# Performance work log

Measured on AMD Instinct MI355X. Metric: run time of the kernel, lower is better.

The kernel has to match this reference:

```python
import jax, jax.numpy as jnp
import numpy as np

H, D = 4, 32  # num_heads, per-head out dim (out_feats=128)
N_AGENT, N_GT, N_UAV = 50000, 50000, 50000
E = 600000
IN = 64


def _gat(x_src, x_dst, src, dst, W_src, W_dst, al, ar, W_res, b, num_dst):
    """DGL-style bipartite GATConv with residual, bias and ReLU activation."""
    fs = (x_src @ W_src).reshape(-1, H, D)      # [Ns,H,D]
    fd = (x_dst @ W_dst).reshape(-1, H, D)      # [Nd,H,D]
    el = jnp.sum(fs * al, axis=-1)              # [Ns,H]
    er = jnp.sum(fd * ar, axis=-1)              # [Nd,H]
    e = jax.nn.leaky_relu(el[src] + er[dst], 0.2)          # [E,H]
    # segment softmax over incoming edges of each dst node
    emax = jax.ops.segment_max(e, dst, num_segments=num_dst)   # [Nd,H], -inf for deg-0
    ee = jnp.exp(e - emax[dst])
    denom = jax.ops.segment_sum(ee, dst, num_segments=num_dst)
    a = ee / denom[dst]                          # [E,H]
    msg = fs[src] * a[:, :, None]                # [E,H,D]
    rst = jax.ops.segment_sum(msg, dst, num_segments=num_dst)  # [Nd,H,D]; zeros for deg-0
    res = (x_dst @ W_res).reshape(-1, H, D)      # residual projection
    out = jax.nn.relu(rst + res + b.reshape(1, H, D))
    return out.reshape(num_dst, H * D)


def setup_inputs() -> dict:
    key = jax.random.key(0)
    ks = jax.random.split(key, 20)
    s = 0.1  # weight init scale
    return {
        'x_gt': jax.random.normal(ks[0], (N_GT, IN), jnp.float32),
        'x_uav': jax.random.normal(ks[1], (N_UAV, IN), jnp.float32),
        'x_agent': jax.random.normal(ks[2], (N_AGENT, IN), jnp.float32),
        'src_gt': jax.random.randint(ks[3], (E,), 0, N_GT, jnp.int32),
        'dst_gt': jax.random.randint(ks[4], (E,), 0, N_AGENT, jnp.int32),
        'src_uav': jax.random.randint(ks[5], (E,), 0, N_UAV, jnp.int32),
        'dst_uav': jax.random.randint(ks[6], (E,), 0, N_AGENT, jnp.int32),
        'W_src_gt': s * jax.random.normal(ks[7], (IN, H * D), jnp.float32),
        'W_dst_gt': s * jax.random.normal(ks[8], (IN, H * D), jnp.float32),
        'attn_l_gt': s * jax.random.normal(ks[9], (H, D), jnp.float32),
        'attn_r_gt': s * jax.random.normal(ks[10], (H, D), jnp.float32),
        'W_res_gt': s * jax.random.normal(ks[11], (IN, H * D), jnp.float32),
        'b_gt': jnp.zeros((H * D,), jnp.float32),
        'W_src_uav': s * jax.random.normal(ks[12], (IN, H * D), jnp.float32),
        'W_dst_uav': s * jax.random.normal(ks[13], (IN, H * D), jnp.float32),
        'attn_l_uav': s * jax.random.normal(ks[14], (H, D), jnp.float32),
        'attn_r_uav': s * jax.random.normal(ks[15], (H, D), jnp.float32),
        'W_res_uav': s * jax.random.normal(ks[16], (IN, H * D), jnp.float32),
        'b_uav': jnp.zeros((H * D,), jnp.float32),
        'W_f': s * jax.random.normal(ks[17], (2 * H * D, H * D), jnp.float32),
        'b_f': jnp.zeros((H * D,), jnp.float32),
    }


def reference(x_gt, x_uav, x_agent, src_gt, dst_gt, src_uav, dst_uav,
              W_src_gt, W_dst_gt, attn_l_gt, attn_r_gt, W_res_gt, b_gt,
              W_src_uav, W_dst_uav, attn_l_uav, attn_r_uav, W_res_uav, b_uav,
              W_f, b_f):
    h_gt = _gat(x_gt, x_agent, src_gt, dst_gt, W_src_gt, W_dst_gt,
                attn_l_gt, attn_r_gt, W_res_gt, b_gt, N_AGENT)
    h_uav = _gat(x_uav, x_agent, src_uav, dst_uav, W_src_uav, W_dst_uav,
                 attn_l_uav, attn_r_uav, W_res_uav, b_uav, N_AGENT)
    h = jnp.concatenate([h_gt, h_uav], axis=1)   # [N_agent, 256]
    return jax.nn.relu(h @ W_f + b_f)            # [N_agent, 128]
```

## Files before the change

kernel.cpp:

```cpp
#include <hip/hip_runtime.h>
#include <hip/hip_bf16.h>

using bf16 = __hip_bfloat16;

#define NA 50000
#define NE 600000

typedef __attribute__((ext_vector_type(8))) short short8;
typedef __attribute__((ext_vector_type(4))) float f32x4;

#define HBUF_B   0u
#define FS_B     25600000u
#define EL_B     51200000u
#define RECS_B   54400000u
#define CNT_B    68800000u
#define ROW_B    72000000u
#define TOPS_B   72400016u
#define FLAG_B   72400528u
#define WST_GT_B 72400544u
#define WST_UAV_B 72416928u
#define WRT_B    72433312u
#define WFT_B    72466080u
#define ELT_GT_B 72531616u
#define ELT_UAV_B 72533664u
#define ERT_B    72535712u
#define RANK_B   72537760u
#define WS_BYTES 77337760u

__device__ __forceinline__ float b2f(bf16 v) { return __bfloat162float(v); }

__device__ __forceinline__ float ldf(const void* p, size_t i, int f32) {
    return f32 ? ((const float*)p)[i] : b2f(((const bf16*)p)[i]);
}

__device__ __forceinline__ unsigned short f2bs(float v) {
    bf16 t = __float2bfloat16(v);
    return *(unsigned short*)&t;
}

__device__ __forceinline__ float lrelu_exp(float v) {
    v = v > 0.f ? v : 0.2f * v;
    return __expf(v);
}

__device__ __forceinline__ unsigned int pack_bf16x2(float a, float b) {
    return (unsigned int)f2bs(a) | ((unsigned int)f2bs(b) << 16);
}

__device__ __forceinline__ float lo_f(unsigned int u) { return __uint_as_float(u << 16); }
__device__ __forceinline__ float hi_f(unsigned int u) { return __uint_as_float(u & 0xffff0000u); }

__device__ __forceinline__ short8 ldfrag8(const void* p, size_t off, int f32) {
    if (!f32) return *(const short8*)((const unsigned short*)p + off);
    union { short8 s; unsigned int u[4]; } r;
    const float* fp = (const float*)p + off;
#pragma unroll
    for (int j = 0; j < 4; ++j) r.u[j] = pack_bf16x2(fp[2 * j], fp[2 * j + 1]);
    return r.s;
}

__device__ __forceinline__ unsigned int xcc_id() {
    unsigned int x;
    asm volatile("s_getreg_b32 %0, hwreg(HW_REG_XCC_ID)" : "=s"(x));
    return x & 7u;
}

__device__ int probe_f32(const void* x0) {
    __shared__ int cnt;
    if (threadIdx.x == 0) cnt = 0;
    __syncthreads();
    const bf16* p = (const bf16*)x0;
    int bad = 0;
    for (int i = threadIdx.x; i < 1024; i += 256) {
        float av = fabsf(b2f(p[i]));
        if (!(av <= 1e6f)) bad++;
    }
    if (bad) atomicAdd(&cnt, bad);
    __syncthreads();
    return cnt > 8;
}

__global__ void HeteroVisionConv_29703993819529_kernel(
    const void* x0,
    const void* Wsg, const void* alg, const void* Wdg, const void* arg_,
    const void* Wsu, const void* alu, const void* Wdu, const void* aru,
    const void* Wrg, const void* Wru, const void* Wf,
    unsigned short* wsT_gt, unsigned short* wsT_uav, unsigned short* wrT,
    unsigned short* wfT, unsigned short* elT_gt, unsigned short* elT_uav,
    unsigned short* erT,
    int* flag, unsigned int* outp, long sent) {
    int b = blockIdx.x, t = threadIdx.x;
    int f32 = probe_f32(x0);
    if (b == 20) {
        if (t == 0) { flag[0] = f32; outp[sent] = 0x447A447Au; }
        return;
    }
    if (b < 8) {
        for (int i = t; i < 16 * 256; i += 256) {
            int n = b * 16 + (i >> 8), k = i & 255;
            wfT[n * 256 + k] = f2bs(ldf(Wf, (size_t)k * 128 + n, f32));
        }
    } else if (b < 12) {
        for (int i = t; i < 64 * 64; i += 256) {
            int n = (b - 8) * 64 + (i >> 6), k = i & 63;
            float v = (n < 128) ? ldf(Wrg, (size_t)k * 128 + n, f32)
                                : ldf(Wru, (size_t)k * 128 + (n - 128), f32);
            wrT[n * 64 + k] = f2bs(v);
        }
    } else if (b < 14) {
        for (int i = t; i < 64 * 64; i += 256) {
            int n = (b - 12) * 64 + (i >> 6), k = i & 63;
            wsT_gt[n * 64 + k] = f2bs(ldf(Wsg, (size_t)k * 128 + n, f32));
        }
    } else if (b < 16) {
        for (int i = t; i < 64 * 64; i += 256) {
            int n = (b - 14) * 64 + (i >> 6), k = i & 63;
            wsT_uav[n * 64 + k] = f2bs(ldf(Wsu, (size_t)k * 128 + n, f32));
        }
    } else {
        int m = b - 16;
        const void* Wm = (m == 0) ? Wsg : (m == 1) ? Wdg : (m == 2) ? Wsu : Wdu;
        const void* Am = (m == 0) ? alg : (m == 1) ? arg_ : (m == 2) ? alu : aru;
        int k = t >> 2, h = t & 3;
        float a = 0.f;
        for (int d = 0; d < 32; ++d)
            a += ldf(Wm, (size_t)k * 128 + h * 32 + d, f32) *
                 ldf(Am, (size_t)h * 32 + d, f32);
        unsigned short v = f2bs(a);
        if (m == 0) {
            elT_gt[h * 64 + k] = v;
            for (int i = t; i < 12 * 64; i += 256) elT_gt[(4 + (i >> 6)) * 64 + (i & 63)] = 0;
        } else if (m == 2) {
            elT_uav[h * 64 + k] = v;
            for (int i = t; i < 12 * 64; i += 256) elT_uav[(4 + (i >> 6)) * 64 + (i & 63)] = 0;
        } else if (m == 1) {
            erT[h * 64 + k] = v;
        } else {
            erT[(4 + h) * 64 + k] = v;
            for (int i = t; i < 8 * 64; i += 256) erT[(8 + (i >> 6)) * 64 + (i & 63)] = 0;
        }
    }
}

__global__ void fused_k(const int* dg, const int* du,
                        unsigned int* cnt, unsigned int* rank,
                        const void* xg, const void* xu, const void* xa,
                        const unsigned short* wsT_gt, const unsigned short* wsT_uav,
                        const unsigned short* elT_gt, const unsigned short* elT_uav,
                        const unsigned short* wrT, const unsigned short* erT,
                        const void* bg, const void* bu,
                        float* elbase, bf16* fs, bf16* hbuf, const int* flag) {
    __shared__ unsigned short Bt[256 * 72];
    __shared__ float bl[256];
    int b = blockIdx.x, t = threadIdx.x;

    if (b < 3516 && (b % 3) == 0) {
        int idx = (b / 3) * 256 + t;
        if (idx >= 300000) return;
        int g = idx >= 150000;
        int e = (idx - g * 150000) * 4;
        int4 d4 = *(const int4*)((g ? du : dg) + e);
        unsigned int xcc = xcc_id();
        unsigned int* c = cnt + xcc * 100000 + g * NA;
        uint4 r4;
        r4.x = __hip_atomic_fetch_add(&c[d4.x], 1u, __ATOMIC_RELAXED,
                                      __HIP_MEMORY_SCOPE_WORKGROUP);
        r4.y = __hip_atomic_fetch_add(&c[d4.y], 1u, __ATOMIC_RELAXED,
                                      __HIP_MEMORY_SCOPE_WORKGROUP);
        r4.z = __hip_atomic_fetch_add(&c[d4.z], 1u, __ATOMIC_RELAXED,
                                      __HIP_MEMORY_SCOPE_WORKGROUP);
        r4.w = __hip_atomic_fetch_add(&c[d4.w], 1u, __ATOMIC_RELAXED,
                                      __HIP_MEMORY_SCOPE_WORKGROUP);
        unsigned int tag = xcc << 24;
        r4.x |= tag; r4.y |= tag; r4.z |= tag; r4.w |= tag;
        *(uint4*)(rank + (size_t)g * NE + e) = r4;
        return;
    }
    int nidx = (b < 3516) ? (b - b / 3 - 1) : (2344 + (b - 3516));
    int f32 = *flag;
    int lane = t & 63, w = t >> 6;
    int m = lane & 15, quad = lane >> 4;

    if (nidx < 1564) {
        int g = nidx / 782, bb = nidx % 782;
        const void* A = g ? xu : xg;
        const unsigned short* WT = g ? wsT_uav : wsT_gt;
        const unsigned short* ET = g ? elT_uav : elT_gt;
        float* elout = elbase + (g ? 400000 : 0);
        bf16* out = fs + (size_t)g * NA * 128;
        for (int i = t * 8; i < 128 * 64; i += 256 * 8) {
            short8 v = *(const short8*)(WT + i);
            int n = i >> 6, k = i & 63;
            *(short8*)&Bt[n * 72 + k] = v;
        }
        __syncthreads();
        int row = bb * 64 + w * 16 + m;
        int rowc = row < NA ? row : NA - 1;
        short8 a0 = ldfrag8(A, (size_t)rowc * 64 + quad * 8, f32);
        short8 a1 = ldfrag8(A, (size_t)rowc * 64 + 32 + quad * 8, f32);
        f32x4 acc[8];
#pragma unroll
        for (int nt = 0; nt < 8; ++nt) acc[nt] = (f32x4){0.f, 0.f, 0.f, 0.f};
#pragma unroll
        for (int nt = 0; nt < 8; ++nt) {
            short8 b0 = *(const short8*)&Bt[(nt * 16 + m) * 72 + quad * 8];
            short8 b1 = *(const short8*)&Bt[(nt * 16 + m) * 72 + 32 + quad * 8];
            acc[nt] = __builtin_amdgcn_mfma_f32_16x16x32_bf16(a0, b0, acc[nt], 0, 0, 0);
            acc[nt] = __builtin_amdgcn_mfma_f32_16x16x32_bf16(a1, b1, acc[nt], 0, 0, 0);
        }
        f32x4 eacc = (f32x4){0.f, 0.f, 0.f, 0.f};
        {
            short8 e0 = *(const short8*)&ET[m * 64 + quad * 8];
            short8 e1 = *(const short8*)&ET[m * 64 + 32 + quad * 8];
            eacc = __builtin_amdgcn_mfma_f32_16x16x32_bf16(a0, e0, eacc, 0, 0, 0);
            eacc = __builtin_amdgcn_mfma_f32_16x16x32_bf16(a1, e1, eacc, 0, 0, 0);
        }
        int srow = bb * 64 + w * 16 + quad * 4;
#pragma unroll
        for (int nt = 0; nt < 8; ++nt) {
#pragma unroll
            for (int r = 0; r < 4; ++r) {
                int rr = srow + r;
                if (rr < NA) out[(size_t)rr * 128 + nt * 16 + m] = __float2bfloat16(acc[nt][r]);
            }
        }
        if (m < 4) {
#pragma unroll
            for (int r = 0; r < 4; ++r) {
                int rr = srow + r;
                if (rr < NA) elout[(size_t)rr * 4 + m] = eacc[r];
            }
        }
        return;
    }
    int bb = nidx - 1564;
    for (int i = t * 8; i < 256 * 64; i += 256 * 8) {
        short8 v = *(const short8*)(wrT + i);
        int n = i >> 6, k = i & 63;
        *(short8*)&Bt[n * 72 + k] = v;
    }
    bl[t] = (t < 128) ? ldf(bg, t, f32) : ldf(bu, t - 128, f32);
    __syncthreads();
    int row = bb * 64 + w * 16 + m;
    int rowc = row < NA ? row : NA - 1;
    short8 a0 = ldfrag8(xa, (size_t)rowc * 64 + quad * 8, f32);
    short8 a1 = ldfrag8(xa, (size_t)rowc * 64 + 32 + quad * 8, f32);
    f32x4 acc[16];
#pragma unroll
    for (int nt = 0; nt < 16; ++nt) acc[nt] = (f32x4){0.f, 0.f, 0.f, 0.f};
#pragma unroll
    for (int nt = 0; nt < 16; ++nt) {
        short8 b0 = *(const short8*)&Bt[(nt * 16 + m) * 72 + quad * 8];
        short8 b1 = *(const short8*)&Bt[(nt * 16 + m) * 72 + 32 + quad * 8];
        acc[nt] = __builtin_amdgcn_mfma_f32_16x16x32_bf16(a0, b0, acc[nt], 0, 0, 0);
        acc[nt] = __builtin_amdgcn_mfma_f32_16x16x32_bf16(a1, b1, acc[nt], 0, 0, 0);
    }
    f32x4 eacc = (f32x4){0.f, 0.f, 0.f, 0.f};
    {
        short8 e0 = *(const short8*)&erT[m * 64 + quad * 8];
        short8 e1 = *(const short8*)&erT[m * 64 + 32 + quad * 8];
        eacc = __builtin_amdgcn_mfma_f32_16x16x32_bf16(a0, e0, eacc, 0, 0, 0);
        eacc = __builtin_amdgcn_mfma_f32_16x16x32_bf16(a1, e1, eacc, 0, 0, 0);
    }
    int srow = bb * 64 + w * 16 + quad * 4;
#pragma unroll
    for (int nt = 0; nt < 16; ++nt) {
        int col = nt * 16 + m;
#pragma unroll
        for (int r = 0; r < 4; ++r) {
            int rr = srow + r;
            if (rr < NA)
                hbuf[(size_t)rr * 256 + col] = __float2bfloat16(acc[nt][r] + bl[col]);
        }
    }
    if (m < 8) {
        float* ero = (m < 4) ? (elbase + 200000) : (elbase + 600000);
        int mm = m & 3;
#pragma unroll
        for (int r = 0; r < 4; ++r) {
            int rr = srow + r;
            if (rr < NA) ero[(size_t)rr * 4 + mm] = eacc[r];
        }
    }
}

__global__ void scan1_k(unsigned int* cnt, unsigned int* row, unsigned int* tops) {
    __shared__ unsigned int sh[256];
    int b = blockIdx.x, t = threadIdx.x;
    int base = b * 1024 + t * 4;
    unsigned int v[4];
    for (int j = 0; j < 4; ++j) {
        int d = base + j;
        unsigned int tot = 0u;
        if (d < 100000) {
#pragma unroll
            for (int x = 0; x < 8; ++x) {
                unsigned int c = cnt[x * 100000 + d];
                cnt[x * 100000 + d] = tot;
                tot += c;
            }
        }
        v[j] = tot;
    }
    unsigned int s = v[0] + v[1] + v[2] + v[3];
    sh[t] = s;
    __syncthreads();
    for (int off = 1; off < 256; off <<= 1) {
        unsigned int x = (t >= off) ? sh[t - off] : 0u;
        __syncthreads();
        sh[t] += x;
        __syncthreads();
    }
    unsigned int run = sh[t] - s;
    for (int j = 0; j < 4; ++j) {
        if (base + j < 100000) row[base + j] = run;
        run += v[j];
    }
    if (t == 255) tops[b] = sh[255];
}

__global__ void scan2_k(unsigned int* tops, unsigned int* row) {
    __shared__ unsigned int sh[128];
    int t = threadIdx.x;
    unsigned int v = (t < 98) ? tops[t] : 0u;
    sh[t] = v;
    __syncthreads();
    for (int off = 1; off < 128; off <<= 1) {
        unsigned int x = (t >= off) ? sh[t - off] : 0u;
        __syncthreads();
        sh[t] += x;
        __syncthreads();
    }
    if (t < 98) tops[t] = sh[t] - v;
    if (t == 97) row[100000] = sh[97];
}

__global__ void scan3_k(unsigned int* row, const unsigned int* tops) {
    int b = blockIdx.x, t = threadIdx.x;
    unsigned int off = tops[b];
    for (int i = b * 1024 + t; i < b * 1024 + 1024; i += 256) {
        if (i < 100000) row[i] += off;
    }
}

__global__ void scatter_k(const int* sg, const int* dg, const int* su, const int* du,
                          const float* elbase, const unsigned int* row,
                          const unsigned int* cnt, const unsigned int* rank,
                          unsigned int* recs) {
    int idx = blockIdx.x * 256 + threadIdx.x;
    if (idx >= 2 * NE) return;
    int g = idx >= NE;
    int e = idx - g * NE;
    int s = (g ? su : sg)[e];
    int d = (g ? du : dg)[e];
    const float4* el4 = (const float4*)(elbase + (g ? 400000 : 0));
    const float4* er4 = (const float4*)(elbase + (g ? 600000 : 200000));
    unsigned int rk = rank[idx];
    unsigned int xcc = rk >> 24, lr = rk & 0xFFFFFFu;
    unsigned int pos = row[g * NA + d] + cnt[xcc * 100000 + g * NA + d] + lr;
    float4 l = el4[s], r = er4[d];
    uint3 rec;
    rec.x = (unsigned int)s;
    rec.y = pack_bf16x2(lrelu_exp(l.x + r.x), lrelu_exp(l.y + r.y));
    rec.z = pack_bf16x2(lrelu_exp(l.z + r.z), lrelu_exp(l.w + r.w));
    *(uint3*)(recs + (size_t)pos * 3) = rec;
}

__global__ void gather_k(const unsigned int* row, const unsigned int* recs,
                         const bf16* fs, bf16* hbuf) {
    int wid = (blockIdx.x * 256 + threadIdx.x) >> 6;
    int lane = threadIdx.x & 63;
    if (wid >= 2 * NA) return;
    int g = wid / NA, d = wid - g * NA;
    int eg = lane >> 4;
    int cl = lane & 15;
    int hsel = cl >> 3;
    int hodd = (cl >> 2) & 1;
    unsigned int start = row[g * NA + d];
    unsigned int end   = row[g * NA + d + 1];
    const uint4* fs4 = (const uint4*)(fs + (size_t)g * NA * 128);

    float denom = 0.f;
    float a[8];
#pragma unroll
    for (int k = 0; k < 8; ++k) a[k] = 0.f;

    if (start < end) {
        uint3 rr[4], rn[4];
#pragma unroll
        for (int j = 0; j < 4; ++j) {
            unsigned int idx = start + 4 * j + eg;
            rr[j] = *(const uint3*)(recs + (size_t)(idx < end ? idx : end - 1) * 3);
        }
        for (unsigned int i = start; i < end; i += 16) {
            uint4 uu[4];
#pragma unroll
            for (int j = 0; j < 4; ++j) uu[j] = fs4[(size_t)rr[j].x * 16 + cl];
            unsigned int inext = i + 16;
#pragma unroll
            for (int j = 0; j < 4; ++j) {
                unsigned int idx = inext + 4 * j + eg;
                rn[j] = *(const uint3*)(recs + (size_t)(idx < end ? idx : end - 1) * 3);
            }
#pragma unroll
            for (int j = 0; j < 4; ++j) {
                unsigned int idx = i + 4 * j + eg;
                unsigned int pp = hsel ? rr[j].z : rr[j].y;
                float e = hodd ? hi_f(pp) : lo_f(pp);
                if (idx >= end) e = 0.f;
                denom += e;
                a[0] += lo_f(uu[j].x) * e;
                a[1] += hi_f(uu[j].x) * e;
                a[2] += lo_f(uu[j].y) * e;
                a[3] += hi_f(uu[j].y) * e;
                a[4] += lo_f(uu[j].z) * e;
                a[5] += hi_f(uu[j].z) * e;
                a[6] += lo_f(uu[j].w) * e;
                a[7] += hi_f(uu[j].w) * e;
            }
#pragma unroll
            for (int j = 0; j < 4; ++j) rr[j] = rn[j];
        }
    }
#pragma unroll
    for (int k = 0; k < 8; ++k) {
        a[k] += __shfl_xor(a[k], 16, 64);
        a[k] += __shfl_xor(a[k], 32, 64);
    }
    denom += __shfl_xor(denom, 16, 64);
    denom += __shfl_xor(denom, 32, 64);
    if (lane < 16) {
        float inv = (end > start) ? 1.f / denom : 0.f;
        uint4* hp = (uint4*)(hbuf + (size_t)d * 256 + g * 128) + cl;
        uint4 rv = *hp;
        float v0 = a[0] * inv + lo_f(rv.x);
        float v1 = a[1] * inv + hi_f(rv.x);
        float v2 = a[2] * inv + lo_f(rv.y);
        float v3 = a[3] * inv + hi_f(rv.y);
        float v4 = a[4] * inv + lo_f(rv.z);
        float v5 = a[5] * inv + hi_f(rv.z);
        float v6 = a[6] * inv + lo_f(rv.w);
        float v7 = a[7] * inv + hi_f(rv.w);
        v0 = v0 > 0.f ? v0 : 0.f;
        v1 = v1 > 0.f ? v1 : 0.f;
        v2 = v2 > 0.f ? v2 : 0.f;
        v3 = v3 > 0.f ? v3 : 0.f;
        v4 = v4 > 0.f ? v4 : 0.f;
        v5 = v5 > 0.f ? v5 : 0.f;
        v6 = v6 > 0.f ? v6 : 0.f;
        v7 = v7 > 0.f ? v7 : 0.f;
        uint4 o;
        o.x = pack_bf16x2(v0, v1);
        o.y = pack_bf16x2(v2, v3);
        o.z = pack_bf16x2(v4, v5);
        o.w = pack_bf16x2(v6, v7);
        *hp = o;
    }
}

__global__ void final_k(const bf16* hbuf, const unsigned short* wfT,
                        const void* bfp, void* outp, const int* flag) {
    int f32 = *flag;
    int b = blockIdx.x;
    __shared__ unsigned short Bt[128 * 72];
    __shared__ float bl[128];
    int t = threadIdx.x;
    if (t < 128) bl[t] = ldf(bfp, t, f32);
    int lane = t & 63, w = t >> 6;
    int m = lane & 15, quad = lane >> 4;
    int row = b * 64 + w * 16 + m;
    int rowc = row < NA ? row : NA - 1;
    f32x4 acc[8];
#pragma unroll
    for (int nt = 0; nt < 8; ++nt) acc[nt] = (f32x4){0.f, 0.f, 0.f, 0.f};
    for (int kc = 0; kc < 4; ++kc) {
        __syncthreads();
        for (int i = t * 8; i < 128 * 64; i += 256 * 8) {
            int n = i >> 6, k = i & 63;
            short8 v = *(const short8*)(wfT + (size_t)n * 256 + kc * 64 + k);
            *(short8*)&Bt[n * 72 + k] = v;
        }
        __syncthreads();
        short8 a0 = *(const short8*)((const unsigned short*)hbuf +
                                     (size_t)rowc * 256 + kc * 64 + quad * 8);
        short8 a1 = *(const short8*)((const unsigned short*)hbuf +
                                     (size_t)rowc * 256 + kc * 64 + 32 + quad * 8);
#pragma unroll
        for (int nt = 0; nt < 8; ++nt) {
            short8 b0 = *(const short8*)&Bt[(nt * 16 + m) * 72 + quad * 8];
            short8 b1 = *(const short8*)&Bt[(nt * 16 + m) * 72 + 32 + quad * 8];
            acc[nt] = __builtin_amdgcn_mfma_f32_16x16x32_bf16(a0, b0, acc[nt], 0, 0, 0);
            acc[nt] = __builtin_amdgcn_mfma_f32_16x16x32_bf16(a1, b1, acc[nt], 0, 0, 0);
        }
    }
    int srow = b * 64 + w * 16 + quad * 4;
#pragma unroll
    for (int nt = 0; nt < 8; ++nt) {
        int col = nt * 16 + m;
        float bv = bl[col];
#pragma unroll
        for (int r = 0; r < 4; ++r) {
            int rr = srow + r;
            if (rr < NA) {
                float v = acc[nt][r] + bv;
                v = v > 0.f ? v : 0.f;
                if (f32) ((float*)outp)[(size_t)rr * 128 + col] = v;
                else ((bf16*)outp)[(size_t)rr * 128 + col] = __float2bfloat16(v);
            }
        }
    }
}

extern "C" void kernel_launch(void* const* d_in, const int* in_sizes, int n_in,
                              void* d_out, int out_size, void* d_ws, size_t ws_size,
                              hipStream_t stream) {
    const void* x_gt     = d_in[0];
    const void* x_uav    = d_in[1];
    const void* x_ag     = d_in[2];
    const int*  src_gt   = (const int*)d_in[3];
    const int*  dst_gt   = (const int*)d_in[4];
    const int*  src_uav  = (const int*)d_in[5];
    const int*  dst_uav  = (const int*)d_in[6];
    const void* Wsrc_gt  = d_in[7];
    const void* Wdst_gt  = d_in[8];
    const void* al_gt    = d_in[9];
    const void* ar_gt    = d_in[10];
    const void* Wres_gt  = d_in[11];
    const void* b_gt     = d_in[12];
    const void* Wsrc_uav = d_in[13];
    const void* Wdst_uav = d_in[14];
    const void* al_uav   = d_in[15];
    const void* ar_uav   = d_in[16];
    const void* Wres_uav = d_in[17];
    const void* b_uav    = d_in[18];
    const void* W_f      = d_in[19];
    const void* b_f      = d_in[20];

    char* wsb = (char*)d_ws;
    bf16* hbuf = (bf16*)(wsb + HBUF_B);
    bf16* fs = (bf16*)(wsb + FS_B);
    float* el = (float*)(wsb + EL_B);
    unsigned int* recs = (unsigned int*)(wsb + RECS_B);
    unsigned int* cnt = (unsigned int*)(wsb + CNT_B);
    unsigned int* row = (unsigned int*)(wsb + ROW_B);
    unsigned int* tops = (unsigned int*)(wsb + TOPS_B);
    int* flag = (int*)(wsb + FLAG_B);
    unsigned short* wsT_gt = (unsigned short*)(wsb + WST_GT_B);
    unsigned short* wsT_uav = (unsigned short*)(wsb + WST_UAV_B);
    unsigned short* wrT = (unsigned short*)(wsb + WRT_B);
    unsigned short* wfT = (unsigned short*)(wsb + WFT_B);
    unsigned short* elT_gt = (unsigned short*)(wsb + ELT_GT_B);
    unsigned short* elT_uav = (unsigned short*)(wsb + ELT_UAV_B);
    unsigned short* erT = (unsigned short*)(wsb + ERT_B);
    unsigned int* rank = (unsigned int*)(wsb + RANK_B);

    if (ws_size < (size_t)WS_BYTES) {
        hipMemsetAsync(d_out, 0x42, (size_t)out_size * 2, stream);
        return;
    }

    long sent = (long)out_size / 2 - 1;

    hipMemsetAsync(cnt, 0, 8 * 100000 * 4, stream);
    HeteroVisionConv_29703993819529_kernel<<<21, 256, 0, stream>>>(
        x_gt, Wsrc_gt, al_gt, Wdst_gt, ar_gt, Wsrc_uav, al_uav, Wdst_uav, ar_uav,
        Wres_gt, Wres_uav, W_f,
        wsT_gt, wsT_uav, wrT, wfT, elT_gt, elT_uav, erT,
        flag, (unsigned int*)d_out, sent);
    fused_k<<<3518, 256, 0, stream>>>(dst_gt, dst_uav, cnt, rank,
                                      x_gt, x_uav, x_ag,
                                      wsT_gt, wsT_uav, elT_gt, elT_uav,
                                      wrT, erT, b_gt, b_uav,
                                      el, fs, hbuf, flag);
    scan1_k<<<98, 256, 0, stream>>>(cnt, row, tops);
    scan2_k<<<1, 128, 0, stream>>>(tops, row);
    scan3_k<<<98, 256, 0, stream>>>(row, tops);
    scatter_k<<<4688, 256, 0, stream>>>(src_gt, dst_gt, src_uav, dst_uav,
                                        el, row, cnt, rank, recs);
    gather_k<<<25000, 256, 0, stream>>>(row, recs, fs, hbuf);
    final_k<<<782, 256, 0, stream>>>(hbuf, wfT, b_f, d_out, flag);
}
```

Baseline: 299.3 us.

## Replace global atomic counting sort with per-chunk LDS byte histograms

Edge destination counting moves from global per-XCC atomics plus a stored rank array to 96 edge chunks, each building an 8-bit packed histogram in LDS and writing it to global memory. The scan then does an exclusive prefix over chunks per bin, and the scatter kernel recomputes each edge's local rank with LDS atomics before writing its record. This drops the memset, the global atomics and the rank buffer, at the cost of extra histogram traffic (96×100K bytes), fewer and larger blocks, and byte counters that overflow if a bin's count within a chunk, or its running count across chunks, exceeds 255.

```diff
diff --git a/kernel.cpp b/kernel.cpp
--- a/kernel.cpp
+++ b/kernel.cpp
@@ -5,6 +5,11 @@
 
 #define NA 50000
 #define NE 600000
+
+#define NCH 96
+#define CHE 12500
+#define HROW 100032
+#define PBINS 33344
 
 typedef __attribute__((ext_vector_type(8))) short short8;
 typedef __attribute__((ext_vector_type(4))) float f32x4;
@@ -13,19 +18,18 @@
 #define FS_B     25600000u
 #define EL_B     51200000u
 #define RECS_B   54400000u
-#define CNT_B    68800000u
-#define ROW_B    72000000u
-#define TOPS_B   72400016u
-#define FLAG_B   72400528u
-#define WST_GT_B 72400544u
-#define WST_UAV_B 72416928u
-#define WRT_B    72433312u
-#define WFT_B    72466080u
-#define ELT_GT_B 72531616u
-#define ELT_UAV_B 72533664u
-#define ERT_B    72535712u
-#define RANK_B   72537760u
-#define WS_BYTES 77337760u
+#define HIST_B   68800000u
+#define ROW_B    78403072u
+#define TOPS_B   78803076u
+#define FLAG_B   78803588u
+#define WST_GT_B 78803600u
+#define WST_UAV_B 78819984u
+#define WRT_B    78836368u
+#define WFT_B    78869136u
+#define ELT_GT_B 78934672u
+#define ELT_UAV_B 78936720u
+#define ERT_B    78938768u
+#define WS_BYTES 78940816u
 
 __device__ __forceinline__ float b2f(bf16 v) { return __bfloat162float(v); }
 
@@ -57,12 +61,6 @@
 #pragma unroll
     for (int j = 0; j < 4; ++j) r.u[j] = pack_bf16x2(fp[2 * j], fp[2 * j + 1]);
     return r.s;
-}
-
-__device__ __forceinline__ unsigned int xcc_id() {
-    unsigned int x;
-    asm volatile("s_getreg_b32 %0, hwreg(HW_REG_XCC_ID)" : "=s"(x));
-    return x & 7u;
 }
 
 __device__ int probe_f32(const void* x0) {
@@ -143,7 +141,7 @@
 }
 
 __global__ void fused_k(const int* dg, const int* du,
-                        unsigned int* cnt, unsigned int* rank,
+                        unsigned char* hist,
                         const void* xg, const void* xu, const void* xa,
                         const unsigned short* wsT_gt, const unsigned short* wsT_uav,
                         const unsigned short* elT_gt, const unsigned short* elT_uav,
@@ -154,29 +152,38 @@
     __shared__ float bl[256];
     int b = blockIdx.x, t = threadIdx.x;
 
-    if (b < 3516 && (b % 3) == 0) {
-        int idx = (b / 3) * 256 + t;
-        if (idx >= 300000) return;
-        int g = idx >= 150000;
-        int e = (idx - g * 150000) * 4;
-        int4 d4 = *(const int4*)((g ? du : dg) + e);
-        unsigned int xcc = xcc_id();
-        unsigned int* c = cnt + xcc * 100000 + g * NA;
-        uint4 r4;
-        r4.x = __hip_atomic_fetch_add(&c[d4.x], 1u, __ATOMIC_RELAXED,
-                                      __HIP_MEMORY_SCOPE_WORKGROUP);
-        r4.y = __hip_atomic_fetch_add(&c[d4.y], 1u, __ATOMIC_RELAXED,
-                                      __HIP_MEMORY_SCOPE_WORKGROUP);
-        r4.z = __hip_atomic_fetch_add(&c[d4.z], 1u, __ATOMIC_RELAXED,
-                                      __HIP_MEMORY_SCOPE_WORKGROUP);
-        r4.w = __hip_atomic_fetch_add(&c[d4.w], 1u, __ATOMIC_RELAXED,
-                                      __HIP_MEMORY_SCOPE_WORKGROUP);
-        unsigned int tag = xcc << 24;
-        r4.x |= tag; r4.y |= tag; r4.z |= tag; r4.w |= tag;
-        *(uint4*)(rank + (size_t)g * NE + e) = r4;
+    if (b < NCH) {
+        int c = b;
+        int g = c >= 48;
+        const int* dp = (g ? du : dg) + (c - g * 48) * CHE;
+        unsigned int* h32 = (unsigned int*)Bt;
+        for (int p = 0; p < 3; ++p) {
+            int binLo = p * PBINS;
+            unsigned int* out = (unsigned int*)(hist + (size_t)c * HROW + binLo);
+            bool live = (binLo + PBINS > g * NA) && (binLo < g * NA + NA);
+            if (!live) {
+                for (int i = t; i < PBINS / 4; i += 256) out[i] = 0u;
+                continue;
+            }
+            for (int i = t; i < PBINS / 4; i += 256) h32[i] = 0u;
+            __syncthreads();
+            for (int i = t; i < CHE / 4; i += 256) {
+                int4 d4 = *(const int4*)(dp + i * 4);
+                int dd[4] = {d4.x, d4.y, d4.z, d4.w};
+#pragma unroll
+                for (int k = 0; k < 4; ++k) {
+                    int rel = g * NA + dd[k] - binLo;
+                    if (rel >= 0 && rel < PBINS)
+                        atomicAdd(&h32[rel >> 2], 1u << (8 * (rel & 3)));
+                }
+            }
+            __syncthreads();
+            for (int i = t; i < PBINS / 4; i += 256) out[i] = h32[i];
+            __syncthreads();
+        }
         return;
     }
-    int nidx = (b < 3516) ? (b - b / 3 - 1) : (2344 + (b - 3516));
+    int nidx = b - NCH;
     int f32 = *flag;
     int lane = t & 63, w = t >> 6;
     int m = lane & 15, quad = lane >> 4;
@@ -284,36 +291,47 @@
     }
 }
 
-__global__ void scan1_k(unsigned int* cnt, unsigned int* row, unsigned int* tops) {
+__global__ void scan1_k(unsigned char* hist, unsigned int* row, unsigned int* tops) {
+    __shared__ unsigned char ch[NCH * 1024];
     __shared__ unsigned int sh[256];
     int b = blockIdx.x, t = threadIdx.x;
-    int base = b * 1024 + t * 4;
+    int base = b * 1024;
+    int off = base + t * 4;
+    for (int c = 0; c < NCH; ++c) {
+        unsigned int w = 0u;
+        if (off + 4 <= HROW) w = *(const unsigned int*)(hist + (size_t)c * HROW + off);
+        *(unsigned int*)&ch[c * 1024 + t * 4] = w;
+    }
+    __syncthreads();
     unsigned int v[4];
     for (int j = 0; j < 4; ++j) {
-        int d = base + j;
-        unsigned int tot = 0u;
-        if (d < 100000) {
-#pragma unroll
-            for (int x = 0; x < 8; ++x) {
-                unsigned int c = cnt[x * 100000 + d];
-                cnt[x * 100000 + d] = tot;
-                tot += c;
-            }
-        }
-        v[j] = tot;
+        int idx = t * 4 + j;
+        unsigned int run = 0;
+        for (int c = 0; c < NCH; ++c) {
+            unsigned int x = ch[c * 1024 + idx];
+            ch[c * 1024 + idx] = (unsigned char)run;
+            run += x;
+        }
+        v[j] = (base + idx < 100000) ? run : 0u;
+    }
+    __syncthreads();
+    for (int c = 0; c < NCH; ++c) {
+        if (off + 4 <= HROW)
+            *(unsigned int*)(hist + (size_t)c * HROW + off) =
+                *(const unsigned int*)&ch[c * 1024 + t * 4];
     }
     unsigned int s = v[0] + v[1] + v[2] + v[3];
     sh[t] = s;
     __syncthreads();
-    for (int off = 1; off < 256; off <<= 1) {
-        unsigned int x = (t >= off) ? sh[t - off] : 0u;
+    for (int o = 1; o < 256; o <<= 1) {
+        unsigned int x = (t >= o) ? sh[t - o] : 0u;
         __syncthreads();
         sh[t] += x;
         __syncthreads();
     }
     unsigned int run = sh[t] - s;
     for (int j = 0; j < 4; ++j) {
-        if (base + j < 100000) row[base + j] = run;
+        if (base + j + t * 4 < 100000) row[base + t * 4 + j] = run;
         run += v[j];
     }
     if (t == 255) tops[b] = sh[255];
@@ -343,27 +361,44 @@
     }
 }
 
-__global__ void scatter_k(const int* sg, const int* dg, const int* su, const int* du,
-                          const float* elbase, const unsigned int* row,
-                          const unsigned int* cnt, const unsigned int* rank,
-                          unsigned int* recs) {
-    int idx = blockIdx.x * 256 + threadIdx.x;
-    if (idx >= 2 * NE) return;
-    int g = idx >= NE;
-    int e = idx - g * NE;
-    int s = (g ? su : sg)[e];
-    int d = (g ? du : dg)[e];
+__global__ void rank_scatter_k(const int* sg, const int* dg, const int* su, const int* du,
+                               const float* elbase, const unsigned int* row,
+                               const unsigned char* hist, unsigned int* recs) {
+    __shared__ unsigned int h32[6252];
+    int b = blockIdx.x, t = threadIdx.x;
+    int c = b >> 2, q = b & 3;
+    int binLo = q * 25008;
+    for (int i = t; i < 6252; i += 256) h32[i] = 0u;
+    __syncthreads();
+    int g = c >= 48;
+    int eoff = (c - g * 48) * CHE;
+    const int* sp = (g ? su : sg) + eoff;
+    const int* dp = (g ? du : dg) + eoff;
     const float4* el4 = (const float4*)(elbase + (g ? 400000 : 0));
     const float4* er4 = (const float4*)(elbase + (g ? 600000 : 200000));
-    unsigned int rk = rank[idx];
-    unsigned int xcc = rk >> 24, lr = rk & 0xFFFFFFu;
-    unsigned int pos = row[g * NA + d] + cnt[xcc * 100000 + g * NA + d] + lr;
-    float4 l = el4[s], r = er4[d];
-    uint3 rec;
-    rec.x = (unsigned int)s;
-    rec.y = pack_bf16x2(lrelu_exp(l.x + r.x), lrelu_exp(l.y + r.y));
-    rec.z = pack_bf16x2(lrelu_exp(l.z + r.z), lrelu_exp(l.w + r.w));
-    *(uint3*)(recs + (size_t)pos * 3) = rec;
+    const unsigned char* cb = hist + (size_t)c * HROW;
+    for (int i = t; i < CHE / 4; i += 256) {
+        int4 s4 = *(const int4*)(sp + i * 4);
+        int4 d4 = *(const int4*)(dp + i * 4);
+        int ss[4] = {s4.x, s4.y, s4.z, s4.w};
+        int dd[4] = {d4.x, d4.y, d4.z, d4.w};
+#pragma unroll
+        for (int k = 0; k < 4; ++k) {
+            int bin = g * NA + dd[k];
+            int rel = bin - binLo;
+            if (rel < 0 || rel >= 25008) continue;
+            unsigned int sh8 = 8u * (rel & 3);
+            unsigned int old = atomicAdd(&h32[rel >> 2], 1u << sh8);
+            unsigned int lr = (old >> sh8) & 255u;
+            unsigned int pos = row[bin] + (unsigned int)cb[bin] + lr;
+            float4 l = el4[ss[k]], r = er4[dd[k]];
+            uint3 rec;
+            rec.x = (unsigned int)ss[k];
+            rec.y = pack_bf16x2(lrelu_exp(l.x + r.x), lrelu_exp(l.y + r.y));
+            rec.z = pack_bf16x2(lrelu_exp(l.z + r.z), lrelu_exp(l.w + r.w));
+            *(uint3*)(recs + (size_t)pos * 3) = rec;
+        }
+    }
 }
 
 __global__ void gather_k(const unsigned int* row, const unsigned int* recs,
@@ -541,7 +576,7 @@
     bf16* fs = (bf16*)(wsb + FS_B);
     float* el = (float*)(wsb + EL_B);
     unsigned int* recs = (unsigned int*)(wsb + RECS_B);
-    unsigned int* cnt = (unsigned int*)(wsb + CNT_B);
+    unsigned char* hist = (unsigned char*)(wsb + HIST_B);
     unsigned int* row = (unsigned int*)(wsb + ROW_B);
     unsigned int* tops = (unsigned int*)(wsb + TOPS_B);
     int* flag = (int*)(wsb + FLAG_B);
@@ -552,7 +587,6 @@
     unsigned short* elT_gt = (unsigned short*)(wsb + ELT_GT_B);
     unsigned short* elT_uav = (unsigned short*)(wsb + ELT_UAV_B);
     unsigned short* erT = (unsigned short*)(wsb + ERT_B);
-    unsigned int* rank = (unsigned int*)(wsb + RANK_B);
 
     if (ws_size < (size_t)WS_BYTES) {
         hipMemsetAsync(d_out, 0x42, (size_t)out_size * 2, stream);
@@ -561,22 +595,21 @@
 
     long sent = (long)out_size / 2 - 1;
 
-    hipMemsetAsync(cnt, 0, 8 * 100000 * 4, stream);
     HeteroVisionConv_29703993819529_kernel<<<21, 256, 0, stream>>>(
         x_gt, Wsrc_gt, al_gt, Wdst_gt, ar_gt, Wsrc_uav, al_uav, Wdst_uav, ar_uav,
         Wres_gt, Wres_uav, W_f,
         wsT_gt, wsT_uav, wrT, wfT, elT_gt, elT_uav, erT,
         flag, (unsigned int*)d_out, sent);
-    fused_k<<<3518, 256, 0, stream>>>(dst_gt, dst_uav, cnt, rank,
-                                      x_gt, x_uav, x_ag,
-                                      wsT_gt, wsT_uav, elT_gt, elT_uav,
-                                      wrT, erT, b_gt, b_uav,
-                                      el, fs, hbuf, flag);
-    scan1_k<<<98, 256, 0, stream>>>(cnt, row, tops);
+    fused_k<<<NCH + 2346, 256, 0, stream>>>(dst_gt, dst_uav, hist,
+                                            x_gt, x_uav, x_ag,
+                                            wsT_gt, wsT_uav, elT_gt, elT_uav,
+                                            wrT, erT, b_gt, b_uav,
+                                            el, fs, hbuf, flag);
+    scan1_k<<<98, 256, 0, stream>>>(hist, row, tops);
     scan2_k<<<1, 128, 0, stream>>>(tops, row);
     scan3_k<<<98, 256, 0, stream>>>(row, tops);
-    scatter_k<<<4688, 256, 0, stream>>>(src_gt, dst_gt, src_uav, dst_uav,
-                                        el, row, cnt, rank, recs);
+    rank_scatter_k<<<NCH * 4, 256, 0, stream>>>(src_gt, dst_gt, src_uav, dst_uav,
+                                                el, row, hist, recs);
     gather_k<<<25000, 256, 0, stream>>>(row, recs, fs, hbuf);
     final_k<<<782, 256, 0, stream>>>(hbuf, wfT, b_f, d_out, flag);
 }
```

Result: slower. 310.5 us (+3.8%).
